# Kernel optimization log

Measured on AMD Instinct MI355X. Metric: run time of the kernel, lower is better.

The kernel has to match this reference:

```python
import jax, jax.numpy as jnp
import numpy as np

B, T, N, D = 16, 1024, 1024, 256   # batch, query len (hp.max_T), key len (hp.max_N), hp.d
WIN = 64                            # hp.attention_win_size
NEG = jnp.float32(-2**32 + 1)       # padding value used by the TF module


def setup_inputs() -> dict:
    key = jax.random.key(0)
    k1, k2, k3, k4 = jax.random.split(key, 4)
    Q = jax.random.normal(k1, (B, T, D), dtype=jnp.float32)
    K = jax.random.normal(k2, (B, N, D), dtype=jnp.float32)
    V = jax.random.normal(k3, (B, N, D), dtype=jnp.float32)
    prev_max_attentions = jax.random.randint(k4, (B,), 0, N - WIN, dtype=jnp.int64)
    return {"Q": Q, "K": K, "V": V, "prev_max_attentions": prev_max_attentions}


def reference(Q, K, V, prev_max_attentions):
    # scaled scores: [B, T, N]
    A = jnp.einsum("btd,bnd->btn", Q, K) * jax.lax.rsqrt(jnp.float32(D))

    # monotonic window mask (mono_attention=True):
    idx = jnp.arange(N)                              # [N]
    prev = prev_max_attentions[:, None]              # [B, 1]
    masks = (idx < prev) | (idx >= prev + WIN)       # [B, N], True = disallowed
    A = jnp.where(masks[:, None, :], NEG, A)         # broadcast over T (== tf.tile)

    A = jax.nn.softmax(A, axis=-1)                   # [B, T, N]
    max_attentions = jnp.argmax(A, axis=-1).astype(jnp.float32)  # [B, T]

    R = jnp.concatenate([jnp.einsum("btn,bnd->btd", A, V), Q], axis=-1)  # [B, T, 2D]
    alignments = jnp.transpose(A, (0, 2, 1))         # [B, N, T]
    return (R, alignments, max_attentions)
```

## Files before the change

kernel.cpp:

```cpp
#include <hip/hip_runtime.h>


#define BB 16
#define TT 1024
#define NN 1024
#define DD 256
#define WIN 64
#define TBLK 16
#define NT 256

#define R_ELEMS   (16u*1024u*512u)
#define ALN_ELEMS (16u*1024u*1024u)

#define LSTR 132

typedef float nt_f4 __attribute__((ext_vector_type(4)));

__device__ __forceinline__ void nt_store4(void* p, float x, float y, float z, float w) {
    nt_f4 v = {x, y, z, w};
    __builtin_nontemporal_store(v, (nt_f4*)p);
}
__device__ __forceinline__ void nt_store4v(void* p, const float4& f) {
    nt_f4 v = {f.x, f.y, f.z, f.w};
    __builtin_nontemporal_store(v, (nt_f4*)p);
}

__global__ __launch_bounds__(NT, 4) void attn_v8(
    const float* __restrict__ Q, const float* __restrict__ K,
    const float* __restrict__ V, const int* __restrict__ prev_in,
    float* __restrict__ out)
{
    __shared__ float ks[WIN * LSTR];
    __shared__ float p_lds[TBLK][WIN + 4];

    float* Rout   = out;
    float* aligns = out + R_ELEMS;
    float* maxatt = out + R_ELEMS + ALN_ELEMS;

    const int tid = threadIdx.x;

    if (blockIdx.x & 1) {
        const int zb    = blockIdx.x >> 1;
        const int b     = zb >> 6;
        const int chunk = zb & 63;
        const int prev  = prev_in[b];
        float* base = aligns + (size_t)b * NN * TT;
        #pragma unroll
        for (int r = 0; r < 15; ++r) {
            int idx = chunk * 15 + r;
            int n   = idx < prev ? idx : idx + WIN;
            nt_store4(base + (size_t)n * TT + tid * 4, 0.f, 0.f, 0.f, 0.f);
        }
        return;
    }

    const int lane = tid & 63;
    const int w    = __builtin_amdgcn_readfirstlane(tid >> 6);
    const int ab   = blockIdx.x >> 1;
    const int b    = ab >> 6;
    const int t0   = (ab & 63) * TBLK;
    const int prev = prev_in[b];

    const float* qb = Q + ((size_t)b * TT + t0 + 4 * w) * DD;

    float acc[4] = {0.f, 0.f, 0.f, 0.f};
    #pragma unroll
    for (int h = 0; h < 2; ++h) {
        if (h) __syncthreads();
        const float4* Ksrc = (const float4*)(K + ((size_t)b * NN + prev) * DD + h * 128);
        #pragma unroll
        for (int k = 0; k < 8; ++k) {
            int t4 = tid + k * NT;
            int r = t4 >> 5, c = t4 & 31;
            float4 v = Ksrc[(size_t)r * 64 + c];
            *(float4*)&ks[r * LSTR + c * 4] = v;
        }
        __syncthreads();

        const float* qh = qb + h * 128;
        #pragma unroll 8
        for (int d4 = 0; d4 < 32; ++d4) {
            float4 kk = *(const float4*)&ks[lane * LSTR + d4 * 4];
            #pragma unroll
            for (int t = 0; t < 4; ++t) {
                float4 q = ((const float4*)(qh + t * DD))[d4];
                acc[t] = fmaf(q.x, kk.x, fmaf(q.y, kk.y, fmaf(q.z, kk.z, fmaf(q.w, kk.w, acc[t]))));
            }
        }
    }

    #pragma unroll
    for (int t = 0; t < 4; ++t) {
        float v = acc[t] * 0.0625f;

        float m = v;
        #pragma unroll
        for (int off = 32; off; off >>= 1) m = fmaxf(m, __shfl_xor(m, off));

        float e = expf(v - m);
        float s = e;
        #pragma unroll
        for (int off = 32; off; off >>= 1) s += __shfl_xor(s, off);

        p_lds[4 * w + t][lane] = e / s;

        float av = v; int ai = lane;
        #pragma unroll
        for (int off = 32; off; off >>= 1) {
            float ov = __shfl_xor(av, off);
            int   oi = __shfl_xor(ai, off);
            if (ov > av || (ov == av && oi < ai)) { av = ov; ai = oi; }
        }
        if (lane == 0) maxatt[(size_t)b * TT + t0 + 4 * w + t] = (float)(prev + ai);
    }
    __syncthreads();

    {
        const int j = tid >> 2, cg = tid & 3;
        nt_store4(aligns + ((size_t)b * NN + prev + j) * TT + t0 + cg * 4,
                  p_lds[cg * 4 + 0][j], p_lds[cg * 4 + 1][j],
                  p_lds[cg * 4 + 2][j], p_lds[cg * 4 + 3][j]);
    }

    {
        const float4* V4 = (const float4*)(V + ((size_t)b * NN + prev) * DD);
        float4 o[4];
        #pragma unroll
        for (int t = 0; t < 4; ++t) o[t] = make_float4(0.f, 0.f, 0.f, 0.f);

        #pragma unroll 4
        for (int j4 = 0; j4 < WIN / 4; ++j4) {
            float4 p0 = *(const float4*)&p_lds[4 * w + 0][j4 * 4];
            float4 p1 = *(const float4*)&p_lds[4 * w + 1][j4 * 4];
            float4 p2 = *(const float4*)&p_lds[4 * w + 2][j4 * 4];
            float4 p3 = *(const float4*)&p_lds[4 * w + 3][j4 * 4];
            float4 v0 = V4[(size_t)(j4 * 4 + 0) * 64 + lane];
            float4 v1 = V4[(size_t)(j4 * 4 + 1) * 64 + lane];
            float4 v2 = V4[(size_t)(j4 * 4 + 2) * 64 + lane];
            float4 v3 = V4[(size_t)(j4 * 4 + 3) * 64 + lane];
            #define ACC4(o_, p_) \
                o_.x = fmaf(p_.x, v0.x, fmaf(p_.y, v1.x, fmaf(p_.z, v2.x, fmaf(p_.w, v3.x, o_.x)))); \
                o_.y = fmaf(p_.x, v0.y, fmaf(p_.y, v1.y, fmaf(p_.z, v2.y, fmaf(p_.w, v3.y, o_.y)))); \
                o_.z = fmaf(p_.x, v0.z, fmaf(p_.y, v1.z, fmaf(p_.z, v2.z, fmaf(p_.w, v3.z, o_.z)))); \
                o_.w = fmaf(p_.x, v0.w, fmaf(p_.y, v1.w, fmaf(p_.z, v2.w, fmaf(p_.w, v3.w, o_.w))));
            ACC4(o[0], p0) ACC4(o[1], p1) ACC4(o[2], p2) ACC4(o[3], p3)
            #undef ACC4
        }

        #pragma unroll
        for (int t = 0; t < 4; ++t) {
            float* Rrow = Rout + ((size_t)b * TT + t0 + 4 * w + t) * (2 * DD);
            nt_store4v(Rrow + lane * 4, o[t]);
            float4 qv = ((const float4*)(qb + t * DD))[lane];
            nt_store4v(Rrow + DD + lane * 4, qv);
        }
    }
}

extern "C" void kernel_launch(void* const* d_in, const int* in_sizes, int n_in,
                              void* d_out, int out_size, void* d_ws, size_t ws_size,
                              hipStream_t stream) {
    const float* Q = (const float*)d_in[0];
    const float* K = (const float*)d_in[1];
    const float* V = (const float*)d_in[2];
    const int* prev = (const int*)d_in[3];
    float* out = (float*)d_out;

    attn_v8<<<2 * (BB * TT / TBLK), NT, 0, stream>>>(Q, K, V, prev, out);
}
```

Baseline: 193.0 us.

## Split zero-fill into separate kernel and use 512-thread blocks with two rows per wave

Moves the zeroing of non-window alignment rows out of the odd blocks of the attention kernel and into its own kernel, launched after the attention kernel. The attention kernel now runs with 512 threads per block, so each of its 8 waves handles 2 query rows instead of 4. This lowers per-thread register and work load and allows more waves in flight. The cost is an extra kernel launch, serialization between the two kernels on the stream, and a little more redundant K staging per row.

```diff
diff --git a/kernel.cpp b/kernel.cpp
--- a/kernel.cpp
+++ b/kernel.cpp
@@ -7,7 +7,7 @@
 #define DD 256
 #define WIN 64
 #define TBLK 16
-#define NT 256
+#define NT 512
 
 #define R_ELEMS   (16u*1024u*512u)
 #define ALN_ELEMS (16u*1024u*1024u)
@@ -25,7 +25,22 @@
     __builtin_nontemporal_store(v, (nt_f4*)p);
 }
 
-__global__ __launch_bounds__(NT, 4) void attn_v8(
+__global__ __launch_bounds__(256) void zero_nonwin(
+    float* __restrict__ aligns, const int* __restrict__ prev_in)
+{
+    const int b     = blockIdx.x >> 6;
+    const int chunk = blockIdx.x & 63;
+    const int prev  = prev_in[b];
+    float* base = aligns + (size_t)b * NN * TT;
+    #pragma unroll
+    for (int r = 0; r < 15; ++r) {
+        int idx = chunk * 15 + r;
+        int n   = idx < prev ? idx : idx + WIN;
+        nt_store4(base + (size_t)n * TT + threadIdx.x * 4, 0.f, 0.f, 0.f, 0.f);
+    }
+}
+
+__global__ __launch_bounds__(NT, 8) void attn_v10(
     const float* __restrict__ Q, const float* __restrict__ K,
     const float* __restrict__ V, const int* __restrict__ prev_in,
     float* __restrict__ out)
@@ -37,39 +52,22 @@
     float* aligns = out + R_ELEMS;
     float* maxatt = out + R_ELEMS + ALN_ELEMS;
 
-    const int tid = threadIdx.x;
-
-    if (blockIdx.x & 1) {
-        const int zb    = blockIdx.x >> 1;
-        const int b     = zb >> 6;
-        const int chunk = zb & 63;
-        const int prev  = prev_in[b];
-        float* base = aligns + (size_t)b * NN * TT;
-        #pragma unroll
-        for (int r = 0; r < 15; ++r) {
-            int idx = chunk * 15 + r;
-            int n   = idx < prev ? idx : idx + WIN;
-            nt_store4(base + (size_t)n * TT + tid * 4, 0.f, 0.f, 0.f, 0.f);
-        }
-        return;
-    }
-
+    const int tid  = threadIdx.x;
     const int lane = tid & 63;
     const int w    = __builtin_amdgcn_readfirstlane(tid >> 6);
-    const int ab   = blockIdx.x >> 1;
-    const int b    = ab >> 6;
-    const int t0   = (ab & 63) * TBLK;
+    const int b    = blockIdx.x >> 6;
+    const int t0   = (blockIdx.x & 63) * TBLK;
     const int prev = prev_in[b];
 
-    const float* qb = Q + ((size_t)b * TT + t0 + 4 * w) * DD;
+    const float* qb = Q + ((size_t)b * TT + t0 + 2 * w) * DD;
 
-    float acc[4] = {0.f, 0.f, 0.f, 0.f};
+    float acc0 = 0.f, acc1 = 0.f;
     #pragma unroll
     for (int h = 0; h < 2; ++h) {
         if (h) __syncthreads();
         const float4* Ksrc = (const float4*)(K + ((size_t)b * NN + prev) * DD + h * 128);
         #pragma unroll
-        for (int k = 0; k < 8; ++k) {
+        for (int k = 0; k < 4; ++k) {
             int t4 = tid + k * NT;
             int r = t4 >> 5, c = t4 & 31;
             float4 v = Ksrc[(size_t)r * 64 + c];
@@ -81,17 +79,17 @@
         #pragma unroll 8
         for (int d4 = 0; d4 < 32; ++d4) {
             float4 kk = *(const float4*)&ks[lane * LSTR + d4 * 4];
-            #pragma unroll
-            for (int t = 0; t < 4; ++t) {
-                float4 q = ((const float4*)(qh + t * DD))[d4];
-                acc[t] = fmaf(q.x, kk.x, fmaf(q.y, kk.y, fmaf(q.z, kk.z, fmaf(q.w, kk.w, acc[t]))));
-            }
+            float4 q0 = ((const float4*)qh)[d4];
+            float4 q1 = ((const float4*)(qh + DD))[d4];
+            acc0 = fmaf(q0.x, kk.x, fmaf(q0.y, kk.y, fmaf(q0.z, kk.z, fmaf(q0.w, kk.w, acc0))));
+            acc1 = fmaf(q1.x, kk.x, fmaf(q1.y, kk.y, fmaf(q1.z, kk.z, fmaf(q1.w, kk.w, acc1))));
         }
     }
 
+    const int tq0 = 2 * w, tq1 = 2 * w + 1;
     #pragma unroll
-    for (int t = 0; t < 4; ++t) {
-        float v = acc[t] * 0.0625f;
+    for (int t = 0; t < 2; ++t) {
+        float v = (t ? acc1 : acc0) * 0.0625f;
 
         float m = v;
         #pragma unroll
@@ -102,7 +100,7 @@
         #pragma unroll
         for (int off = 32; off; off >>= 1) s += __shfl_xor(s, off);
 
-        p_lds[4 * w + t][lane] = e / s;
+        p_lds[2 * w + t][lane] = e / s;
 
         float av = v; int ai = lane;
         #pragma unroll
@@ -111,11 +109,11 @@
             int   oi = __shfl_xor(ai, off);
             if (ov > av || (ov == av && oi < ai)) { av = ov; ai = oi; }
         }
-        if (lane == 0) maxatt[(size_t)b * TT + t0 + 4 * w + t] = (float)(prev + ai);
+        if (lane == 0) maxatt[(size_t)b * TT + t0 + 2 * w + t] = (float)(prev + ai);
     }
     __syncthreads();
 
-    {
+    if (tid < 256) {
         const int j = tid >> 2, cg = tid & 3;
         nt_store4(aligns + ((size_t)b * NN + prev + j) * TT + t0 + cg * 4,
                   p_lds[cg * 4 + 0][j], p_lds[cg * 4 + 1][j],
@@ -124,16 +122,13 @@
 
     {
         const float4* V4 = (const float4*)(V + ((size_t)b * NN + prev) * DD);
-        float4 o[4];
-        #pragma unroll
-        for (int t = 0; t < 4; ++t) o[t] = make_float4(0.f, 0.f, 0.f, 0.f);
+        float4 o0 = make_float4(0.f, 0.f, 0.f, 0.f);
+        float4 o1 = make_float4(0.f, 0.f, 0.f, 0.f);
 
         #pragma unroll 4
         for (int j4 = 0; j4 < WIN / 4; ++j4) {
-            float4 p0 = *(const float4*)&p_lds[4 * w + 0][j4 * 4];
-            float4 p1 = *(const float4*)&p_lds[4 * w + 1][j4 * 4];
-            float4 p2 = *(const float4*)&p_lds[4 * w + 2][j4 * 4];
-            float4 p3 = *(const float4*)&p_lds[4 * w + 3][j4 * 4];
+            float4 p0 = *(const float4*)&p_lds[tq0][j4 * 4];
+            float4 p1 = *(const float4*)&p_lds[tq1][j4 * 4];
             float4 v0 = V4[(size_t)(j4 * 4 + 0) * 64 + lane];
             float4 v1 = V4[(size_t)(j4 * 4 + 1) * 64 + lane];
             float4 v2 = V4[(size_t)(j4 * 4 + 2) * 64 + lane];
@@ -143,17 +138,18 @@
                 o_.y = fmaf(p_.x, v0.y, fmaf(p_.y, v1.y, fmaf(p_.z, v2.y, fmaf(p_.w, v3.y, o_.y)))); \
                 o_.z = fmaf(p_.x, v0.z, fmaf(p_.y, v1.z, fmaf(p_.z, v2.z, fmaf(p_.w, v3.z, o_.z)))); \
                 o_.w = fmaf(p_.x, v0.w, fmaf(p_.y, v1.w, fmaf(p_.z, v2.w, fmaf(p_.w, v3.w, o_.w))));
-            ACC4(o[0], p0) ACC4(o[1], p1) ACC4(o[2], p2) ACC4(o[3], p3)
+            ACC4(o0, p0) ACC4(o1, p1)
             #undef ACC4
         }
 
-        #pragma unroll
-        for (int t = 0; t < 4; ++t) {
-            float* Rrow = Rout + ((size_t)b * TT + t0 + 4 * w + t) * (2 * DD);
-            nt_store4v(Rrow + lane * 4, o[t]);
-            float4 qv = ((const float4*)(qb + t * DD))[lane];
-            nt_store4v(Rrow + DD + lane * 4, qv);
-        }
+        float* Rrow0 = Rout + ((size_t)b * TT + t0 + tq0) * (2 * DD);
+        float* Rrow1 = Rrow0 + 2 * DD;
+        nt_store4v(Rrow0 + lane * 4, o0);
+        nt_store4v(Rrow1 + lane * 4, o1);
+        float4 q0 = ((const float4*)qb)[lane];
+        float4 q1 = ((const float4*)(qb + DD))[lane];
+        nt_store4v(Rrow0 + DD + lane * 4, q0);
+        nt_store4v(Rrow1 + DD + lane * 4, q1);
     }
 }
 
@@ -166,5 +162,6 @@
     const int* prev = (const int*)d_in[3];
     float* out = (float*)d_out;
 
-    attn_v8<<<2 * (BB * TT / TBLK), NT, 0, stream>>>(Q, K, V, prev, out);
+    attn_v10<<<BB * TT / TBLK, NT, 0, stream>>>(Q, K, V, prev, out);
+    zero_nonwin<<<1024, 256, 0, stream>>>(out + R_ELEMS, prev);
 }
```

After: 179.3 us. -7.1%, faster.
